# Performance work log

Hardware: AMD Instinct MI355X
Metric: run time of the kernel (lower is better)

## Reference

```python
import jax, jax.numpy as jnp
import numpy as np

B = 32        # decode batch (one new token per sequence)
S = 4096      # kv cache length per sequence
H = 32        # query heads
G = 2         # kv groups (multi-query groups)
D = 128       # head dim (kv_channels)
ROT = D // 2  # rotary dim = 64, is_neox_style=False (GPT-J interleaved)
HID = 4096    # hidden size
QKV = (H + 2 * G) * D  # 4608
BASE = 10000.0


def setup_inputs() -> dict:
    key = jax.random.key(0)
    ks = jax.random.split(key, 7)
    return {
        "hidden_states": jax.random.normal(ks[0], (B, HID), jnp.float32),
        "positions": jax.random.randint(ks[1], (B,), 0, S, jnp.int32),
        "k_cache": jax.random.normal(ks[2], (B, S, G, D), jnp.float32) * 0.5,
        "v_cache": jax.random.normal(ks[3], (B, S, G, D), jnp.float32) * 0.5,
        "W_qkv": jax.random.normal(ks[4], (HID, QKV), jnp.float32) * 0.02,
        "b_qkv": jax.random.normal(ks[5], (QKV,), jnp.float32) * 0.02,
        "W_dense": jax.random.normal(ks[6], (H * D, HID), jnp.float32) * 0.02,
    }


def _apply_rope(x, pos):
    # x: [b, n_heads, D]; GPT-J style interleaved rotation on first ROT dims
    inv_freq = 1.0 / (BASE ** (jnp.arange(0, ROT, 2, dtype=jnp.float32) / ROT))  # [ROT//2]
    freqs = pos[:, None].astype(jnp.float32) * inv_freq                          # [b, ROT//2]
    cos = jnp.cos(freqs)[:, None, :]
    sin = jnp.sin(freqs)[:, None, :]
    xr, xp = x[..., :ROT], x[..., ROT:]
    x1, x2 = xr[..., 0::2], xr[..., 1::2]
    o1 = x1 * cos - x2 * sin
    o2 = x2 * cos + x1 * sin
    rot = jnp.stack([o1, o2], axis=-1).reshape(x.shape[:-1] + (ROT,))
    return jnp.concatenate([rot, xp], axis=-1)


def reference(hidden_states, positions, k_cache, v_cache, W_qkv, b_qkv, W_dense):
    # fused QKV projection (MQA split: H query heads, G kv groups)
    qkv = hidden_states @ W_qkv + b_qkv                     # [B, QKV]
    q = qkv[:, : H * D].reshape(B, H, D)
    k = qkv[:, H * D : (H + G) * D].reshape(B, G, D)
    v = qkv[:, (H + G) * D :].reshape(B, G, D)

    # inline RoPE on q and new k
    q = _apply_rope(q, positions)
    k = _apply_rope(k, positions)

    # write new k/v into cache at the current position (paged-cache write)
    b_idx = jnp.arange(B)
    kc = k_cache.at[b_idx, positions].set(k)                # [B, S, G, D]
    vc = v_cache.at[b_idx, positions].set(v)

    # grouped-query attention over the cache, causal via context length
    scale = jnp.float32(D) ** -0.5
    qg = q.reshape(B, G, H // G, D)                         # map head h -> group h // (H/G)
    logits = jnp.einsum("bghd,bsgd->bghs", qg, kc) * scale  # [B, G, H/G, S]
    valid = jnp.arange(S)[None, :] <= positions[:, None]    # [B, S]
    logits = jnp.where(valid[:, None, None, :], logits, jnp.float32(-1e9))
    probs = jax.nn.softmax(logits, axis=-1)
    ctx = jnp.einsum("bghs,bsgd->bghd", probs, vc).reshape(B, H * D)

    return ctx @ W_dense                                    # [B, HID]
```

## Files before the change

### kernel.cpp

```cpp
#include <hip/hip_runtime.h>
#include <math.h>

#define Bz 32
#define Sz 4096
#define Hz 32
#define Gz 2
#define Dz 128
#define HIDz 4096
#define QKVz 4608
#define NCHc 16

static __device__ __forceinline__ void fma4(float4& a, float s, const float4& v) {
  a.x = fmaf(s, v.x, a.x);
  a.y = fmaf(s, v.y, a.y);
  a.z = fmaf(s, v.z, a.z);
  a.w = fmaf(s, v.w, a.w);
}
static __device__ __forceinline__ float dot4(const float4& a, const float4& b, float acc) {
  return fmaf(a.x, b.x, fmaf(a.y, b.y, fmaf(a.z, b.z, fmaf(a.w, b.w, acc))));
}

__global__ __launch_bounds__(256) void gemm_partial(
    const float* __restrict__ X, const float* __restrict__ W,
    float* __restrict__ part, int K, int N, int KH) {
  extern __shared__ float hl[];
  const int stride = KH + 4;
  const int t = threadIdx.x;
  const int k0 = blockIdx.y * KH;
  const int cols4 = KH >> 2;
  const int total4 = Bz * cols4;
  for (int fi = t; fi < total4; fi += 256) {
    const int row = fi / cols4;
    const int c4 = fi - row * cols4;
    const float4 v = *(const float4*)&X[(size_t)row * K + k0 + c4 * 4];
    *(float4*)&hl[row * stride + c4 * 4] = v;
  }
  __syncthreads();
  const int jl = t & 31;
  const int b0 = (t >> 5) * 4;
  const int j = blockIdx.x * 128 + jl * 4;
  float4 acc[4];
  #pragma unroll
  for (int i = 0; i < 4; i++) acc[i] = make_float4(0.f, 0.f, 0.f, 0.f);
  #pragma unroll 4
  for (int kk = 0; kk < KH; kk += 4) {
    const float4 w0 = *(const float4*)&W[(size_t)(k0 + kk + 0) * N + j];
    const float4 w1 = *(const float4*)&W[(size_t)(k0 + kk + 1) * N + j];
    const float4 w2 = *(const float4*)&W[(size_t)(k0 + kk + 2) * N + j];
    const float4 w3 = *(const float4*)&W[(size_t)(k0 + kk + 3) * N + j];
    #pragma unroll
    for (int bi = 0; bi < 4; bi++) {
      const float4 hb = *(const float4*)&hl[(b0 + bi) * stride + kk];
      fma4(acc[bi], hb.x, w0);
      fma4(acc[bi], hb.y, w1);
      fma4(acc[bi], hb.z, w2);
      fma4(acc[bi], hb.w, w3);
    }
  }
  #pragma unroll
  for (int bi = 0; bi < 4; bi++) {
    *(float4*)&part[((size_t)blockIdx.y * Bz + b0 + bi) * N + j] = acc[bi];
  }
}

__global__ __launch_bounds__(256) void qkv_finish(
    const float* __restrict__ part, const float* __restrict__ bias,
    const int* __restrict__ positions, int KT,
    float* __restrict__ qrot, float* __restrict__ krot, float* __restrict__ vnew) {
  const int t = threadIdx.x;
  const int b = blockIdx.x;
  const int head = blockIdx.y * 4 + (t >> 6);
  const int tp = t & 63;
  const int j0 = head * Dz + tp * 2;
  float s0 = bias[j0];
  float s1 = bias[j0 + 1];
  for (int kt = 0; kt < KT; kt++) {
    const float2 p = *(const float2*)&part[((size_t)kt * Bz + b) * QKVz + j0];
    s0 += p.x;
    s1 += p.y;
  }
  float o0 = s0, o1 = s1;
  if (head < Hz + Gz && tp < 32) {
    const float invf = exp2f(-(float)tp * (13.287712379549449f / 32.0f));
    const float a = (float)positions[b] * invf;
    float sn, cs;
    sincosf(a, &sn, &cs);
    o0 = s0 * cs - s1 * sn;
    o1 = s1 * cs + s0 * sn;
  }
  if (head < Hz) {
    const float sc = 0.08838834764831845f;
    float2 o = make_float2(o0 * sc, o1 * sc);
    *(float2*)&qrot[((size_t)b * Hz + head) * Dz + tp * 2] = o;
  } else if (head < Hz + Gz) {
    float2 o = make_float2(o0, o1);
    *(float2*)&krot[((size_t)b * Gz + (head - Hz)) * Dz + tp * 2] = o;
  } else {
    float2 o = make_float2(s0, s1);
    *(float2*)&vnew[((size_t)b * Gz + (head - Hz - Gz)) * Dz + tp * 2] = o;
  }
}

__global__ __launch_bounds__(256, 2) void attn_unit(
    const float* __restrict__ qrot, const float* __restrict__ kcache,
    const float* __restrict__ vcache, const float* __restrict__ krot,
    const float* __restrict__ vnew, const int* __restrict__ positions,
    float* __restrict__ mbuf, float* __restrict__ lbuf, float* __restrict__ pacc) {
  __shared__ float kb[2][32 * 128];
  __shared__ float vb[2][32 * 128];
  __shared__ float ml[128];
  const int g = blockIdx.y, b = blockIdx.z, bx = blockIdx.x;
  const int pos = positions[b];
  const int lt = pos + 1;
  const int blo = (bx * lt) >> 4;
  const int bhi = ((bx + 1) * lt) >> 4;
  const int ntile = (bhi - blo + 31) >> 5;
  const int t = threadIdx.x;
  const int w = t >> 6, lane = t & 63;
  const int h = lane >> 2, dq = lane & 3;

  float4 qr[8];
  {
    const float* qsrc = &qrot[((size_t)b * Hz + g * 16 + h) * Dz + dq * 32];
    #pragma unroll
    for (int j = 0; j < 8; ++j) qr[j] = *(const float4*)&qsrc[j * 4];
  }
  const float* krow_new = &krot[((size_t)b * Gz + g) * Dz];
  const float* vrow_new = &vnew[((size_t)b * Gz + g) * Dz];
  const size_t kvb = ((size_t)b * Sz) * (Gz * Dz) + (size_t)g * Dz;

  const int rr0 = t >> 5, c16 = t & 31;
  float4 sk[4], sv[4];
#define LOADT(tile)                                                              \
  { _Pragma("unroll") for (int r4 = 0; r4 < 4; ++r4) {                           \
      const int sg = blo + (tile) * 32 + rr0 + r4 * 8;                           \
      const float* kp = (sg >= bhi || sg == pos) ? krow_new                      \
                         : &kcache[kvb + (size_t)sg * (Gz * Dz)];                \
      const float* vp = (sg >= bhi || sg == pos) ? vrow_new                      \
                         : &vcache[kvb + (size_t)sg * (Gz * Dz)];                \
      sk[r4] = *(const float4*)&kp[c16 * 4];                                     \
      sv[r4] = *(const float4*)&vp[c16 * 4]; } }
#define WRITET(buf)                                                              \
  { _Pragma("unroll") for (int r4 = 0; r4 < 4; ++r4) {                           \
      *(float4*)&kb[buf][(rr0 + r4 * 8) * 128 + c16 * 4] = sk[r4];               \
      *(float4*)&vb[buf][(rr0 + r4 * 8) * 128 + c16 * 4] = sv[r4]; } }

  float m_run = -1e30f, l_run = 0.f;
  float4 A[8];
  #pragma unroll
  for (int j = 0; j < 8; ++j) A[j] = make_float4(0.f, 0.f, 0.f, 0.f);

  int cur = 0;
  if (ntile > 0) {
    LOADT(0);
    WRITET(0);
    __syncthreads();
  }
  for (int tile = 0; tile < ntile; ++tile) {
    if (tile + 1 < ntile) LOADT(tile + 1);
    const int nvr = bhi - (blo + tile * 32 + w * 8);
    if (nvr > 0) {
      float lg[8];
      #pragma unroll
      for (int s8 = 0; s8 < 8; ++s8) {
        const float* kRow = &kb[cur][(w * 8 + s8) * 128 + dq * 32];
        float a0 = 0.f, a1 = 0.f, a2 = 0.f, a3 = 0.f;
        #pragma unroll
        for (int jj = 0; jj < 2; ++jj) {
          const float4 k0 = *(const float4*)&kRow[(jj * 4 + 0) * 4];
          const float4 k1 = *(const float4*)&kRow[(jj * 4 + 1) * 4];
          const float4 k2 = *(const float4*)&kRow[(jj * 4 + 2) * 4];
          const float4 k3 = *(const float4*)&kRow[(jj * 4 + 3) * 4];
          a0 = dot4(qr[jj * 4 + 0], k0, a0);
          a1 = dot4(qr[jj * 4 + 1], k1, a1);
          a2 = dot4(qr[jj * 4 + 2], k2, a2);
          a3 = dot4(qr[jj * 4 + 3], k3, a3);
        }
        float acc = (a0 + a1) + (a2 + a3);
        acc += __shfl_xor(acc, 1);
        acc += __shfl_xor(acc, 2);
        lg[s8] = acc;
      }
      float tm = -1e30f;
      #pragma unroll
      for (int s8 = 0; s8 < 8; ++s8) tm = fmaxf(tm, (s8 < nvr) ? lg[s8] : -1e30f);
      const float mn = fmaxf(m_run, tm);
      const float sc = __expf(m_run - mn);
      m_run = mn;
      l_run *= sc;
      #pragma unroll
      for (int j = 0; j < 8; ++j) {
        A[j].x *= sc; A[j].y *= sc; A[j].z *= sc; A[j].w *= sc;
      }
      float ps = 0.f;
      #pragma unroll
      for (int s8 = 0; s8 < 8; ++s8) {
        const float p = (s8 < nvr) ? __expf(lg[s8] - mn) : 0.f;
        lg[s8] = p;
        ps += p;
      }
      l_run += ps;
      #pragma unroll
      for (int s8 = 0; s8 < 8; ++s8) {
        const float* vRow = &vb[cur][(w * 8 + s8) * 128 + dq * 32];
        const float p = lg[s8];
        #pragma unroll
        for (int j = 0; j < 8; ++j) {
          const float4 vv = *(const float4*)&vRow[j * 4];
          fma4(A[j], p, vv);
        }
      }
    }
    if (tile + 1 < ntile) {
      WRITET(cur ^ 1);
      __syncthreads();
      cur ^= 1;
    }
  }

  __syncthreads();
  if (dq == 0) {
    ml[w * 32 + h] = m_run;
    ml[w * 32 + 16 + h] = l_run;
  }
  __syncthreads();
  const float ms = fmaxf(fmaxf(ml[h], ml[32 + h]), fmaxf(ml[64 + h], ml[96 + h]));
  const float ew = __expf(m_run - ms);
  float* Aw = kb[0];
  for (int step = 0; step < 4; ++step) {
    if (w == step) {
      #pragma unroll
      for (int j = 0; j < 8; ++j) {
        float4 x;
        if (step == 0) {
          x = make_float4(ew * A[j].x, ew * A[j].y, ew * A[j].z, ew * A[j].w);
        } else {
          x = *(const float4*)&Aw[h * 132 + dq * 32 + j * 4];
          fma4(x, ew, A[j]);
        }
        *(float4*)&Aw[h * 132 + dq * 32 + j * 4] = x;
      }
    }
    __syncthreads();
  }
  const size_t cb = (size_t)(b * Gz + g) * NCHc + bx;
  for (int o = t; o < 512; o += 256) {
    const int hh = o >> 5, d4c = o & 31;
    *(float4*)&pacc[cb * 2048 + (size_t)hh * Dz + d4c * 4] =
        *(const float4*)&Aw[hh * 132 + d4c * 4];
  }
  if (t < 16) {
    const int hh = t;
    const float m0 = ml[hh], m1 = ml[32 + hh], m2 = ml[64 + hh], m3 = ml[96 + hh];
    const float msf = fmaxf(fmaxf(m0, m1), fmaxf(m2, m3));
    const float l = __expf(m0 - msf) * ml[16 + hh] + __expf(m1 - msf) * ml[48 + hh] +
                    __expf(m2 - msf) * ml[80 + hh] + __expf(m3 - msf) * ml[112 + hh];
    mbuf[cb * 16 + hh] = msf;
    lbuf[cb * 16 + hh] = l;
  }
#undef LOADT
#undef WRITET
}

__global__ __launch_bounds__(512) void attn_combine(
    const float* __restrict__ mbuf, const float* __restrict__ lbuf,
    const float* __restrict__ pacc, const int* __restrict__ positions,
    float* __restrict__ ctx) {
  const int bg = blockIdx.x;
  const int b = bg >> 1, g = bg & 1;
  const int t = threadIdx.x;
  const int h = t >> 5, dg = t & 31;
  const size_t mlb = (size_t)bg * NCHc * 16 + h;
  float mstar = -1e30f;
  for (int c = 0; c < NCHc; c++) mstar = fmaxf(mstar, mbuf[mlb + c * 16]);
  float lsum = 0.f;
  float4 A = make_float4(0.f, 0.f, 0.f, 0.f);
  for (int c = 0; c < NCHc; c++) {
    const float wv = __expf(mbuf[mlb + c * 16] - mstar);
    lsum += wv * lbuf[mlb + c * 16];
    const float4 p = *(const float4*)&pacc[((size_t)bg * NCHc + c) * 2048 + (size_t)h * Dz + dg * 4];
    fma4(A, wv, p);
  }
  const float inv = 1.0f / lsum;
  float4 o = make_float4(A.x * inv, A.y * inv, A.z * inv, A.w * inv);
  *(float4*)&ctx[(size_t)b * (Hz * Dz) + (g * 16 + h) * Dz + dg * 4] = o;
}

__global__ __launch_bounds__(256) void reduce_out(
    const float* __restrict__ part, float* __restrict__ out, int KT) {
  const int idx = blockIdx.x * 256 + threadIdx.x;
  const int b = idx >> 12;
  const int j = idx & 4095;
  float s = 0.f;
  for (int kt = 0; kt < KT; kt++) s += part[((size_t)kt * Bz + b) * HIDz + j];
  out[idx] = s;
}

extern "C" void kernel_launch(void* const* d_in, const int* in_sizes, int n_in,
                              void* d_out, int out_size, void* d_ws, size_t ws_size,
                              hipStream_t stream) {
  const float* hidden = (const float*)d_in[0];
  const int* positions = (const int*)d_in[1];
  const float* kcache = (const float*)d_in[2];
  const float* vcache = (const float*)d_in[3];
  const float* Wqkv = (const float*)d_in[4];
  const float* bqkv = (const float*)d_in[5];
  const float* Wd = (const float*)d_in[6];
  float* out = (float*)d_out;

  auto need = [](int KT) -> size_t {
    return (size_t)KT * Bz * QKVz
         + (size_t)Bz * Hz * Dz
         + (size_t)Bz * Gz * Dz * 2
         + (size_t)Bz * Gz * NCHc * 16 * 2
         + (size_t)Bz * Gz * NCHc * 2048
         + (size_t)Bz * HIDz;
  };
  int KT = 32;
  if (need(32) * sizeof(float) > ws_size) KT = 16;
  const int KH = HIDz / KT;

  float* w = (float*)d_ws;
  float* p1 = w;    w += (size_t)KT * Bz * QKVz;
  float* qrot = w;  w += (size_t)Bz * Hz * Dz;
  float* krot = w;  w += (size_t)Bz * Gz * Dz;
  float* vnew = w;  w += (size_t)Bz * Gz * Dz;
  float* mbuf = w;  w += (size_t)Bz * Gz * NCHc * 16;
  float* lbuf = w;  w += (size_t)Bz * Gz * NCHc * 16;
  float* pacc = w;  w += (size_t)Bz * Gz * NCHc * 2048;
  float* ctx = w;

  const size_t smem = (size_t)Bz * (KH + 4) * sizeof(float);

  gemm_partial<<<dim3(QKVz / 128, KT), 256, smem, stream>>>(hidden, Wqkv, p1, HIDz, QKVz, KH);
  qkv_finish<<<dim3(Bz, 9), 256, 0, stream>>>(p1, bqkv, positions, KT, qrot, krot, vnew);
  attn_unit<<<dim3(NCHc, Gz, Bz), 256, 0, stream>>>(qrot, kcache, vcache, krot, vnew, positions,
                                                    mbuf, lbuf, pacc);
  attn_combine<<<dim3(Bz * Gz), 512, 0, stream>>>(mbuf, lbuf, pacc, positions, ctx);
  gemm_partial<<<dim3(HIDz / 128, KT), 256, smem, stream>>>(ctx, Wd, p1, Hz * Dz, HIDz, KH);
  reduce_out<<<dim3(Bz * HIDz / 256), 256, 0, stream>>>(p1, out, KT);
}
```

Baseline: 169.2 us.

## Stage KV tiles via global_load_lds and remap attention threads to rows

New measurement: 169.6 us. No clear change (+0.3%).

```diff
diff --git a/kernel.cpp b/kernel.cpp
--- a/kernel.cpp
+++ b/kernel.cpp
@@ -18,6 +18,11 @@
 }
 static __device__ __forceinline__ float dot4(const float4& a, const float4& b, float acc) {
   return fmaf(a.x, b.x, fmaf(a.y, b.y, fmaf(a.z, b.z, fmaf(a.w, b.w, acc))));
+}
+static __device__ __forceinline__ void gload16(const float* src, float* ldst) {
+  __builtin_amdgcn_global_load_lds(
+      (const __attribute__((address_space(1))) void*)src,
+      (__attribute__((address_space(3))) void*)ldst, 16, 0, 0);
 }
 
 __global__ __launch_bounds__(256) void gemm_partial(
@@ -106,139 +111,164 @@
     const float* __restrict__ vcache, const float* __restrict__ krot,
     const float* __restrict__ vnew, const int* __restrict__ positions,
     float* __restrict__ mbuf, float* __restrict__ lbuf, float* __restrict__ pacc) {
-  __shared__ float kb[2][32 * 128];
-  __shared__ float vb[2][32 * 128];
+  __shared__ float kb[2][4096];
+  __shared__ float vb[2][4096];
+  __shared__ float qt[2176];
+  __shared__ float pl[4][160];
   __shared__ float ml[128];
   const int g = blockIdx.y, b = blockIdx.z, bx = blockIdx.x;
   const int pos = positions[b];
   const int lt = pos + 1;
   const int blo = (bx * lt) >> 4;
   const int bhi = ((bx + 1) * lt) >> 4;
-  const int ntile = (bhi - blo + 31) >> 5;
+  const int nr = bhi - blo;
+  const int ntile = (nr + 31) >> 5;
   const int t = threadIdx.x;
   const int w = t >> 6, lane = t & 63;
-  const int h = lane >> 2, dq = lane & 3;
-
-  float4 qr[8];
-  {
-    const float* qsrc = &qrot[((size_t)b * Hz + g * 16 + h) * Dz + dq * 32];
-    #pragma unroll
-    for (int j = 0; j < 8; ++j) qr[j] = *(const float4*)&qsrc[j * 4];
-  }
+  const int s8 = lane >> 3, c8 = lane & 7;
+
+  for (int i = t; i < 512; i += 256) {
+    const int c = i >> 4, h = i & 15;
+    const float4 q = *(const float4*)&qrot[((size_t)b * Hz + g * 16 + h) * Dz + c * 4];
+    *(float4*)&qt[c * 68 + h * 4] = q;
+  }
+
   const float* krow_new = &krot[((size_t)b * Gz + g) * Dz];
   const float* vrow_new = &vnew[((size_t)b * Gz + g) * Dz];
   const size_t kvb = ((size_t)b * Sz) * (Gz * Dz) + (size_t)g * Dz;
 
-  const int rr0 = t >> 5, c16 = t & 31;
-  float4 sk[4], sv[4];
-#define LOADT(tile)                                                              \
-  { _Pragma("unroll") for (int r4 = 0; r4 < 4; ++r4) {                           \
-      const int sg = blo + (tile) * 32 + rr0 + r4 * 8;                           \
-      const float* kp = (sg >= bhi || sg == pos) ? krow_new                      \
-                         : &kcache[kvb + (size_t)sg * (Gz * Dz)];                \
-      const float* vp = (sg >= bhi || sg == pos) ? vrow_new                      \
-                         : &vcache[kvb + (size_t)sg * (Gz * Dz)];                \
-      sk[r4] = *(const float4*)&kp[c16 * 4];                                     \
-      sv[r4] = *(const float4*)&vp[c16 * 4]; } }
-#define WRITET(buf)                                                              \
-  { _Pragma("unroll") for (int r4 = 0; r4 < 4; ++r4) {                           \
-      *(float4*)&kb[buf][(rr0 + r4 * 8) * 128 + c16 * 4] = sk[r4];               \
-      *(float4*)&vb[buf][(rr0 + r4 * 8) * 128 + c16 * 4] = sv[r4]; } }
-
-  float m_run = -1e30f, l_run = 0.f;
-  float4 A[8];
+#define STAGE(tile, buf)                                                          \
+  { _Pragma("unroll") for (int r4 = 0; r4 < 4; ++r4) {                            \
+      const int sg = blo + (tile) * 32 + r4 * 8 + (t >> 5);                       \
+      const bool fresh = (sg >= bhi) || (sg == pos);                              \
+      const float* kp = fresh ? krow_new : &kcache[kvb + (size_t)sg * (Gz * Dz)]; \
+      const float* vp = fresh ? vrow_new : &vcache[kvb + (size_t)sg * (Gz * Dz)]; \
+      gload16(kp + (t & 31) * 4, &kb[buf][r4 * 1024 + t * 4]);                    \
+      gload16(vp + (t & 31) * 4, &vb[buf][r4 * 1024 + t * 4]); } }
+
+  float m_run[16], l_run[16];
+  float2 A2[16];
   #pragma unroll
-  for (int j = 0; j < 8; ++j) A[j] = make_float4(0.f, 0.f, 0.f, 0.f);
+  for (int h = 0; h < 16; ++h) {
+    m_run[h] = -1e30f;
+    l_run[h] = 0.f;
+    A2[h] = make_float2(0.f, 0.f);
+  }
 
   int cur = 0;
-  if (ntile > 0) {
-    LOADT(0);
-    WRITET(0);
+  if (ntile > 0) STAGE(0, 0);
+  __syncthreads();
+
+  for (int tile = 0; tile < ntile; ++tile) {
+    if (tile + 1 < ntile) STAGE(tile + 1, cur ^ 1);
+    const int rbase = tile * 32 + w * 8;
+    const bool valid = (rbase + s8) < nr;
+
+    float lp[16];
+    #pragma unroll
+    for (int h = 0; h < 16; ++h) lp[h] = 0.f;
+    float4 kf[4];
+    #pragma unroll
+    for (int it = 0; it < 4; ++it)
+      kf[it] = *(const float4*)&kb[cur][(w * 8 + s8) * 128 + (c8 + it * 8) * 4];
+    #pragma unroll
+    for (int it = 0; it < 4; ++it) {
+      #pragma unroll
+      for (int h = 0; h < 16; ++h) {
+        const float4 qv = *(const float4*)&qt[(c8 + it * 8) * 68 + h * 4];
+        lp[h] = dot4(qv, kf[it], lp[h]);
+      }
+    }
+    #pragma unroll
+    for (int h = 0; h < 16; ++h) {
+      lp[h] += __shfl_xor(lp[h], 1);
+      lp[h] += __shfl_xor(lp[h], 2);
+      lp[h] += __shfl_xor(lp[h], 4);
+    }
+    #pragma unroll
+    for (int h = 0; h < 16; ++h) {
+      const float lg = valid ? lp[h] : -1e30f;
+      float v = lg;
+      v = fmaxf(v, __shfl_xor(v, 8));
+      v = fmaxf(v, __shfl_xor(v, 16));
+      v = fmaxf(v, __shfl_xor(v, 32));
+      const float mn = fmaxf(m_run[h], v);
+      const float sc = __expf(m_run[h] - mn);
+      m_run[h] = mn;
+      const float p = valid ? __expf(lg - mn) : 0.f;
+      float ts = p;
+      ts += __shfl_xor(ts, 8);
+      ts += __shfl_xor(ts, 16);
+      ts += __shfl_xor(ts, 32);
+      l_run[h] = l_run[h] * sc + ts;
+      A2[h].x *= sc;
+      A2[h].y *= sc;
+      lp[h] = p;
+    }
+    if (c8 == 0) {
+      float* pr = &pl[w][s8 * 20];
+      *(float4*)&pr[0] = make_float4(lp[0], lp[1], lp[2], lp[3]);
+      *(float4*)&pr[4] = make_float4(lp[4], lp[5], lp[6], lp[7]);
+      *(float4*)&pr[8] = make_float4(lp[8], lp[9], lp[10], lp[11]);
+      *(float4*)&pr[12] = make_float4(lp[12], lp[13], lp[14], lp[15]);
+    }
+    #pragma unroll
+    for (int s = 0; s < 8; ++s) {
+      const float2 v2 = *(const float2*)&vb[cur][(w * 8 + s) * 128 + lane * 2];
+      const float4 p0 = *(const float4*)&pl[w][s * 20 + 0];
+      const float4 p1 = *(const float4*)&pl[w][s * 20 + 4];
+      const float4 p2 = *(const float4*)&pl[w][s * 20 + 8];
+      const float4 p3 = *(const float4*)&pl[w][s * 20 + 12];
+      A2[0].x = fmaf(p0.x, v2.x, A2[0].x);  A2[0].y = fmaf(p0.x, v2.y, A2[0].y);
+      A2[1].x = fmaf(p0.y, v2.x, A2[1].x);  A2[1].y = fmaf(p0.y, v2.y, A2[1].y);
+      A2[2].x = fmaf(p0.z, v2.x, A2[2].x);  A2[2].y = fmaf(p0.z, v2.y, A2[2].y);
+      A2[3].x = fmaf(p0.w, v2.x, A2[3].x);  A2[3].y = fmaf(p0.w, v2.y, A2[3].y);
+      A2[4].x = fmaf(p1.x, v2.x, A2[4].x);  A2[4].y = fmaf(p1.x, v2.y, A2[4].y);
+      A2[5].x = fmaf(p1.y, v2.x, A2[5].x);  A2[5].y = fmaf(p1.y, v2.y, A2[5].y);
+      A2[6].x = fmaf(p1.z, v2.x, A2[6].x);  A2[6].y = fmaf(p1.z, v2.y, A2[6].y);
+      A2[7].x = fmaf(p1.w, v2.x, A2[7].x);  A2[7].y = fmaf(p1.w, v2.y, A2[7].y);
+      A2[8].x = fmaf(p2.x, v2.x, A2[8].x);  A2[8].y = fmaf(p2.x, v2.y, A2[8].y);
+      A2[9].x = fmaf(p2.y, v2.x, A2[9].x);  A2[9].y = fmaf(p2.y, v2.y, A2[9].y);
+      A2[10].x = fmaf(p2.z, v2.x, A2[10].x); A2[10].y = fmaf(p2.z, v2.y, A2[10].y);
+      A2[11].x = fmaf(p2.w, v2.x, A2[11].x); A2[11].y = fmaf(p2.w, v2.y, A2[11].y);
+      A2[12].x = fmaf(p3.x, v2.x, A2[12].x); A2[12].y = fmaf(p3.x, v2.y, A2[12].y);
+      A2[13].x = fmaf(p3.y, v2.x, A2[13].x); A2[13].y = fmaf(p3.y, v2.y, A2[13].y);
+      A2[14].x = fmaf(p3.z, v2.x, A2[14].x); A2[14].y = fmaf(p3.z, v2.y, A2[14].y);
+      A2[15].x = fmaf(p3.w, v2.x, A2[15].x); A2[15].y = fmaf(p3.w, v2.y, A2[15].y);
+    }
     __syncthreads();
-  }
-  for (int tile = 0; tile < ntile; ++tile) {
-    if (tile + 1 < ntile) LOADT(tile + 1);
-    const int nvr = bhi - (blo + tile * 32 + w * 8);
-    if (nvr > 0) {
-      float lg[8];
-      #pragma unroll
-      for (int s8 = 0; s8 < 8; ++s8) {
-        const float* kRow = &kb[cur][(w * 8 + s8) * 128 + dq * 32];
-        float a0 = 0.f, a1 = 0.f, a2 = 0.f, a3 = 0.f;
-        #pragma unroll
-        for (int jj = 0; jj < 2; ++jj) {
-          const float4 k0 = *(const float4*)&kRow[(jj * 4 + 0) * 4];
-          const float4 k1 = *(const float4*)&kRow[(jj * 4 + 1) * 4];
-          const float4 k2 = *(const float4*)&kRow[(jj * 4 + 2) * 4];
-          const float4 k3 = *(const float4*)&kRow[(jj * 4 + 3) * 4];
-          a0 = dot4(qr[jj * 4 + 0], k0, a0);
-          a1 = dot4(qr[jj * 4 + 1], k1, a1);
-          a2 = dot4(qr[jj * 4 + 2], k2, a2);
-          a3 = dot4(qr[jj * 4 + 3], k3, a3);
-        }
-        float acc = (a0 + a1) + (a2 + a3);
-        acc += __shfl_xor(acc, 1);
-        acc += __shfl_xor(acc, 2);
-        lg[s8] = acc;
-      }
-      float tm = -1e30f;
-      #pragma unroll
-      for (int s8 = 0; s8 < 8; ++s8) tm = fmaxf(tm, (s8 < nvr) ? lg[s8] : -1e30f);
-      const float mn = fmaxf(m_run, tm);
-      const float sc = __expf(m_run - mn);
-      m_run = mn;
-      l_run *= sc;
-      #pragma unroll
-      for (int j = 0; j < 8; ++j) {
-        A[j].x *= sc; A[j].y *= sc; A[j].z *= sc; A[j].w *= sc;
-      }
-      float ps = 0.f;
-      #pragma unroll
-      for (int s8 = 0; s8 < 8; ++s8) {
-        const float p = (s8 < nvr) ? __expf(lg[s8] - mn) : 0.f;
-        lg[s8] = p;
-        ps += p;
-      }
-      l_run += ps;
-      #pragma unroll
-      for (int s8 = 0; s8 < 8; ++s8) {
-        const float* vRow = &vb[cur][(w * 8 + s8) * 128 + dq * 32];
-        const float p = lg[s8];
-        #pragma unroll
-        for (int j = 0; j < 8; ++j) {
-          const float4 vv = *(const float4*)&vRow[j * 4];
-          fma4(A[j], p, vv);
-        }
-      }
-    }
-    if (tile + 1 < ntile) {
-      WRITET(cur ^ 1);
-      __syncthreads();
-      cur ^= 1;
-    }
-  }
-
+    cur ^= 1;
+  }
+
+  if (lane == 0) {
+    #pragma unroll
+    for (int h = 0; h < 16; h += 4) {
+      *(float4*)&ml[w * 32 + h] = make_float4(m_run[h], m_run[h + 1], m_run[h + 2], m_run[h + 3]);
+      *(float4*)&ml[w * 32 + 16 + h] =
+          make_float4(l_run[h], l_run[h + 1], l_run[h + 2], l_run[h + 3]);
+    }
+  }
   __syncthreads();
-  if (dq == 0) {
-    ml[w * 32 + h] = m_run;
-    ml[w * 32 + 16 + h] = l_run;
-  }
-  __syncthreads();
-  const float ms = fmaxf(fmaxf(ml[h], ml[32 + h]), fmaxf(ml[64 + h], ml[96 + h]));
-  const float ew = __expf(m_run - ms);
+  float ew[16];
+  #pragma unroll
+  for (int h = 0; h < 16; ++h) {
+    const float ms = fmaxf(fmaxf(ml[h], ml[32 + h]), fmaxf(ml[64 + h], ml[96 + h]));
+    ew[h] = __expf(m_run[h] - ms);
+  }
   float* Aw = kb[0];
   for (int step = 0; step < 4; ++step) {
     if (w == step) {
       #pragma unroll
-      for (int j = 0; j < 8; ++j) {
-        float4 x;
+      for (int h = 0; h < 16; ++h) {
+        float2 x;
         if (step == 0) {
-          x = make_float4(ew * A[j].x, ew * A[j].y, ew * A[j].z, ew * A[j].w);
+          x = make_float2(ew[h] * A2[h].x, ew[h] * A2[h].y);
         } else {
-          x = *(const float4*)&Aw[h * 132 + dq * 32 + j * 4];
-          fma4(x, ew, A[j]);
+          x = *(const float2*)&Aw[h * 132 + lane * 2];
+          x.x = fmaf(ew[h], A2[h].x, x.x);
+          x.y = fmaf(ew[h], A2[h].y, x.y);
         }
-        *(float4*)&Aw[h * 132 + dq * 32 + j * 4] = x;
+        *(float2*)&Aw[h * 132 + lane * 2] = x;
       }
     }
     __syncthreads();
@@ -258,8 +288,7 @@
     mbuf[cb * 16 + hh] = msf;
     lbuf[cb * 16 + hh] = l;
   }
-#undef LOADT
-#undef WRITET
+#undef STAGE
 }
 
 __global__ __launch_bounds__(512) void attn_combine(
```
